# Optimization experiments

Measured on AMD Instinct MI355X. Metric: run time of the kernel, lower is better.

The kernel has to match this reference:

```python
import jax, jax.numpy as jnp
import numpy as np

N = 50000      # num nodes
IN = 256       # in_channels
H = 4          # heads
C = 64         # out_channels per head (concat=False -> out_dim = C)
HOPS = 3       # max_hops == num hops provided
E = 400000     # edges per hop
NEG_SLOPE = 0.2


def setup_inputs() -> dict:
    key = jax.random.key(0)
    ks = jax.random.split(key, 10)
    s_in = 1.0 / np.sqrt(IN)
    s_c = 1.0 / np.sqrt(C)
    return {
        "x": jax.random.normal(ks[0], (N, IN), jnp.float32),
        "ei0": jax.random.randint(ks[1], (2, E), 0, N, dtype=jnp.int32),
        "ei1": jax.random.randint(ks[2], (2, E), 0, N, dtype=jnp.int32),
        "ei2": jax.random.randint(ks[3], (2, E), 0, N, dtype=jnp.int32),
        # shared left/right projections (lin_l / lin_r, shared across hops)
        "W_l": jax.random.normal(ks[4], (IN, H * C), jnp.float32) * s_in,
        "b_l": jnp.zeros((H * C,), jnp.float32),
        "W_r": jax.random.normal(ks[5], (IN, H * C), jnp.float32) * s_in,
        "b_r": jnp.zeros((H * C,), jnp.float32),
        # hop-specific attention vectors and output biases
        "att": jax.random.normal(ks[6], (HOPS, H, C), jnp.float32) * s_c,
        "bias": jnp.zeros((HOPS, C), jnp.float32),
        # hop gate (single Linear since gate_hidden=None)
        "W_gate": jax.random.normal(ks[7], (IN, HOPS), jnp.float32) * s_in,
        "b_gate": jnp.zeros((HOPS,), jnp.float32),
    }


def _segment_softmax(logits, seg, n):
    # logits: [E, H], seg: [E] destination node ids
    m = jax.ops.segment_max(logits, seg, num_segments=n)          # [N, H]
    m = jnp.where(jnp.isfinite(m), m, 0.0)                        # empty segments -> 0
    ex = jnp.exp(logits - m[seg])
    s = jax.ops.segment_sum(ex, seg, num_segments=n)              # [N, H]
    return ex / (s[seg] + 1e-16)


def _gatv2_hop(x_l, x_r, edge_index, att_k, bias_k):
    # x_l, x_r: [N, H, C] shared projections; edge_index: [2, Ek]
    src, dst = edge_index[0], edge_index[1]
    s = jax.nn.leaky_relu(x_l[src] + x_r[dst], NEG_SLOPE)         # [Ek, H, C]
    alpha = jnp.einsum("ehc,hc->eh", s, att_k)                    # [Ek, H]
    alpha = _segment_softmax(alpha, dst, N)
    msg = jax.ops.segment_sum(x_l[src] * alpha[..., None], dst, num_segments=N)  # [N, H, C]
    return msg.mean(axis=1) + bias_k                              # concat=False -> head mean, [N, C]


def reference(x, ei0, ei1, ei2, W_l, b_l, W_r, b_r, att, bias, W_gate, b_gate):
    # shared projections computed once
    x_l = (x @ W_l + b_l).reshape(N, H, C)
    x_r = (x @ W_r + b_r).reshape(N, H, C)

    # hop 0 gets self-loops (add_self_loops=True); higher hops do not
    ar = jnp.arange(N, dtype=ei0.dtype)
    ei0_sl = jnp.concatenate([ei0, jnp.stack([ar, ar])], axis=1)
    edges = [ei0_sl, ei1, ei2]

    messages = jnp.stack(
        [_gatv2_hop(x_l, x_r, edges[k], att[k], bias[k]) for k in range(HOPS)],
        axis=1,
    )  # [N, HOPS, C]

    logits = x @ W_gate + b_gate                                  # [N, HOPS]
    weights = jax.nn.softmax(logits, axis=-1)
    out = jnp.einsum("nkc,nk->nc", messages, weights)             # [N, C]
    return out
```

## Files before the change

kernel.cpp:

```cpp
#include <hip/hip_runtime.h>
#include <math.h>

#define N_NODES 50000
#define IN_DIM 256
#define HEADS 4
#define CDIM 64
#define HC 256
#define HOPS 3
#define EDGES 400000
#define NEG_SLOPE 0.2f
#define SEG (EDGES + N_NODES)
#define TOT_E (3 * EDGES + N_NODES)
#define CAP 32
#define LOG2E 1.44269504f

#define NB_GATE  ((N_NODES + 3) / 4)
#define NB_PACKW ((IN_DIM * 2 * HC) / 256)
#define NB_ZERO  ((HOPS * N_NODES + 255) / 256)
#define NB_SCAT  ((TOT_E + 255) / 256)
#define GB 64
#define AP 264
#define GEMM_BLKS  ((N_NODES + GB - 1) / GB)
#define FUSED_BLKS (GEMM_BLKS + NB_SCAT)

typedef unsigned short ushort;
using short8  = __attribute__((ext_vector_type(8))) short;
using floatx4 = __attribute__((ext_vector_type(4))) float;
using f32x2   = __attribute__((ext_vector_type(2))) float;

__device__ __forceinline__ void decode_flat(int f, int& k, int& e)
{
    if (f < SEG)              { k = 0; e = f; }
    else if (f < SEG + EDGES) { k = 1; e = f - SEG; }
    else                      { k = 2; e = f - SEG - EDGES; }
}

__device__ __forceinline__ ushort f2bf(float f)
{
    unsigned u = __float_as_uint(f);
    unsigned r = u + 0x7fffu + ((u >> 16) & 1u);
    return (ushort)(r >> 16);
}

__device__ __forceinline__ float exp2_raw(float x)
{
    float r;
    asm volatile("v_exp_f32 %0, %1" : "=v"(r) : "v"(x));
    return r;
}

template <int CTRL>
__device__ __forceinline__ float dpp_xadd(float x)
{
    int y = __builtin_amdgcn_update_dpp(
        0, __float_as_int(x), CTRL, 0xF, 0xF, true);
    return x + __int_as_float(y);
}
#define DPP_XOR1 0xB1
#define DPP_XOR2 0x4E
#define DPP_HMIR 0x141

__device__ __forceinline__ f32x2 bf2x(unsigned u)
{
    f32x2 r;
    r.x = __uint_as_float(u << 16);
    r.y = __uint_as_float(u & 0xffff0000u);
    return r;
}

__device__ __forceinline__ f32x2 lrelu2(f32x2 v)
{
    return __builtin_elementwise_max(v, 0.2f * v);
}

__global__ __launch_bounds__(256) void prep_a(
    const float* __restrict__ X, const float* __restrict__ Wg,
    const float* __restrict__ bg, float* __restrict__ gw,
    ushort* __restrict__ Xb,
    const float* __restrict__ Wl, const float* __restrict__ Wr,
    ushort* __restrict__ WT, int* __restrict__ cnt)
{
    const int blk = blockIdx.x;
    const int tid = threadIdx.x;

    if (blk < NB_GATE) {
        const int node = (blk * 256 + tid) >> 6;
        const int lane = tid & 63;
        if (node >= N_NODES) return;

        float4 xv = ((const float4*)(X + (size_t)node * IN_DIM))[lane];

        union { ushort s[4]; uint2 u; } o;
        o.s[0] = f2bf(xv.x); o.s[1] = f2bf(xv.y);
        o.s[2] = f2bf(xv.z); o.s[3] = f2bf(xv.w);
        ((uint2*)(Xb + (size_t)node * IN_DIM))[lane] = o.u;

        float a0 = 0.f, a1 = 0.f, a2 = 0.f;
        const int i0 = lane * 4;
        a0 += xv.x * Wg[(i0 + 0) * HOPS + 0]; a1 += xv.x * Wg[(i0 + 0) * HOPS + 1]; a2 += xv.x * Wg[(i0 + 0) * HOPS + 2];
        a0 += xv.y * Wg[(i0 + 1) * HOPS + 0]; a1 += xv.y * Wg[(i0 + 1) * HOPS + 1]; a2 += xv.y * Wg[(i0 + 1) * HOPS + 2];
        a0 += xv.z * Wg[(i0 + 2) * HOPS + 0]; a1 += xv.z * Wg[(i0 + 2) * HOPS + 1]; a2 += xv.z * Wg[(i0 + 2) * HOPS + 2];
        a0 += xv.w * Wg[(i0 + 3) * HOPS + 0]; a1 += xv.w * Wg[(i0 + 3) * HOPS + 1]; a2 += xv.w * Wg[(i0 + 3) * HOPS + 2];

        #pragma unroll
        for (int off = 32; off >= 1; off >>= 1) {
            a0 += __shfl_xor(a0, off);
            a1 += __shfl_xor(a1, off);
            a2 += __shfl_xor(a2, off);
        }
        if (lane == 0) {
            float l0 = a0 + bg[0], l1 = a1 + bg[1], l2 = a2 + bg[2];
            float m = fmaxf(l0, fmaxf(l1, l2));
            float e0 = expf(l0 - m), e1 = expf(l1 - m), e2 = expf(l2 - m);
            float inv = 1.f / (e0 + e1 + e2);
            gw[node * HOPS + 0] = e0 * inv;
            gw[node * HOPS + 1] = e1 * inv;
            gw[node * HOPS + 2] = e2 * inv;
        }
    } else if (blk < NB_GATE + NB_PACKW) {
        int id = (blk - NB_GATE) * 256 + tid;
        int n = id >> 8;
        int k = id & 255;
        float v = (n < HC) ? Wl[k * HC + n] : Wr[k * HC + (n - HC)];
        WT[(size_t)n * IN_DIM + k] = f2bf(v);
    } else {
        int id = (blk - NB_GATE - NB_PACKW) * 256 + tid;
        if (id < HOPS * N_NODES) cnt[id] = 0;
    }
}

__global__ __launch_bounds__(256, 2) void gemm_scatter(
    const ushort* __restrict__ Xb, const ushort* __restrict__ WT,
    const float* __restrict__ b_l, const float* __restrict__ b_r,
    ushort* __restrict__ xlb, ushort* __restrict__ xrb, int M,
    const int* __restrict__ ei0, const int* __restrict__ ei1,
    const int* __restrict__ ei2, int* __restrict__ cnt,
    ushort* __restrict__ bucket)
{
    __shared__ ushort As[GB][AP];
    const int blk = blockIdx.x;
    const int tid = threadIdx.x;

    if (blk >= GEMM_BLKS) {
        int f = (blk - GEMM_BLKS) * 256 + tid;
        if (f >= TOT_E) return;
        int k, e; decode_flat(f, k, e);
        int s, d;
        if (k == 0 && e >= EDGES) { s = d = e - EDGES; }
        else {
            const int* ei = (k == 0) ? ei0 : (k == 1) ? ei1 : ei2;
            s = ei[e]; d = ei[EDGES + e];
        }
        int pos = atomicAdd(&cnt[k * N_NODES + d], 1);
        if (pos < CAP)
            bucket[((size_t)k * N_NODES + d) * CAP + pos] = (ushort)s;
        return;
    }

    const int wave = tid >> 6, lane = tid & 63;
    const int row0 = blk * GB;
    const int wx   = wave * 128;
    const int lrow = lane & 15, lk = (lane >> 4) * 8;

    #pragma unroll
    for (int j = 0; j < 8; j++) {
        int id = tid + 256 * j;
        int r  = id >> 5;
        int c  = (id & 31) * 8;
        int gr = row0 + r;
        uint4 v = make_uint4(0u, 0u, 0u, 0u);
        if (gr < M)
            v = *(const uint4*)(Xb + (size_t)gr * IN_DIM + c);
        *(uint4*)&As[r][c] = v;
    }
    __syncthreads();

    floatx4 acc[4][8];
    #pragma unroll
    for (int i = 0; i < 4; i++)
        #pragma unroll
        for (int j = 0; j < 8; j++)
            acc[i][j] = (floatx4){0.f, 0.f, 0.f, 0.f};

    #pragma unroll 2
    for (int k0 = 0; k0 < IN_DIM; k0 += 32) {
        short8 af[4], bf[8];
        #pragma unroll
        for (int ni = 0; ni < 8; ni++)
            bf[ni] = *(const short8*)(WT +
                (size_t)(wx + ni * 16 + lrow) * IN_DIM + k0 + lk);
        #pragma unroll
        for (int mi = 0; mi < 4; mi++)
            af[mi] = *(const short8*)&As[mi * 16 + lrow][k0 + lk];

        #pragma unroll
        for (int mi = 0; mi < 4; mi++)
            #pragma unroll
            for (int ni = 0; ni < 8; ni++)
                acc[mi][ni] = __builtin_amdgcn_mfma_f32_16x16x32_bf16(
                    bf[ni], af[mi], acc[mi][ni], 0, 0, 0);
    }

    const int csub = (lane >> 4) * 4;
    const bool left = (wx < HC);
    const float*  bvec = left ? b_l : b_r;
    ushort*       obuf = left ? xlb : xrb;
    const int     cbase = left ? wx : wx - HC;
    #pragma unroll
    for (int mi = 0; mi < 4; mi++) {
        int grow = row0 + mi * 16 + lrow;
        if (grow < M) {
            #pragma unroll
            for (int ni = 0; ni < 8; ni++) {
                int lc = cbase + ni * 16 + csub;
                floatx4 v = acc[mi][ni];
                const float4 b = *(const float4*)(bvec + lc);
                union { ushort s[4]; uint2 u; } o;
                o.s[0] = f2bf(v[0] + b.x);
                o.s[1] = f2bf(v[1] + b.y);
                o.s[2] = f2bf(v[2] + b.z);
                o.s[3] = f2bf(v[3] + b.w);
                *(uint2*)(obuf + (size_t)grow * HC + lc) = o.u;
            }
        }
    }
}

__global__ __launch_bounds__(192) void node_all(
    const ushort* __restrict__ xlb, const ushort* __restrict__ xrb,
    const int* __restrict__ cnt, const ushort* __restrict__ bucket,
    const float* __restrict__ att, const float* __restrict__ gw,
    const float* __restrict__ bias, float* __restrict__ out)
{
    __shared__ float lds[HOPS][CDIM];
    const int n    = blockIdx.x;
    const int k    = threadIdx.x >> 6;
    const int lane = threadIdx.x & 63;
    const int half = lane >> 5;
    const int sub  = lane & 31;
    const unsigned laneoff = (unsigned)sub * 8;

    const int deg = min(cnt[k * N_NODES + n], CAP);
    const ushort* bk = bucket + ((size_t)k * N_NODES + n) * CAP;

    uint4 rq = *(const uint4*)(xrb + (size_t)n * HC + laneoff);
    f32x2 rr[4] = { bf2x(rq.x), bf2x(rq.y), bf2x(rq.z), bf2x(rq.w) };

    const float4 a0 = ((const float4*)(att + (size_t)k * HC))[sub * 2 + 0];
    const float4 a1 = ((const float4*)(att + (size_t)k * HC))[sub * 2 + 1];
    f32x2 w2[4] = { {a0.x * LOG2E, a0.y * LOG2E}, {a0.z * LOG2E, a0.w * LOG2E},
                    {a1.x * LOG2E, a1.y * LOG2E}, {a1.z * LOG2E, a1.w * LOG2E} };

    float denom = 0.f;
    f32x2 acc2[4] = { {0.f,0.f}, {0.f,0.f}, {0.f,0.f}, {0.f,0.f} };

    if (deg > 0) {
        const int degm1 = deg - 1;
        int myS = (lane < deg) ? (int)bk[lane] : 0;
        const int npair = (deg + 1) >> 1;

        int s0 = __shfl(myS, min(half, degm1));
        uint4 q = *(const uint4*)(xlb + (unsigned)s0 * HC + laneoff);

        for (int j = 0; j < npair; j++) {
            int sn = __shfl(myS, min(2 * (j + 1) + half, degm1));
            uint4 qn = *(const uint4*)(xlb + (unsigned)sn * HC + laneoff);

            f32x2 f0 = bf2x(q.x), f1 = bf2x(q.y);
            f32x2 f2 = bf2x(q.z), f3 = bf2x(q.w);

            f32x2 pp = w2[0] * lrelu2(f0 + rr[0]);
            pp = __builtin_elementwise_fma(w2[1], lrelu2(f1 + rr[1]), pp);
            pp = __builtin_elementwise_fma(w2[2], lrelu2(f2 + rr[2]), pp);
            pp = __builtin_elementwise_fma(w2[3], lrelu2(f3 + rr[3]), pp);
            float p = pp.x + pp.y;

            p = dpp_xadd<DPP_XOR1>(p);
            p = dpp_xadd<DPP_XOR2>(p);
            p = dpp_xadd<DPP_HMIR>(p);

            bool valid = (2 * j + half) < deg;
            float ex = valid ? exp2_raw(p) : 0.f;
            denom += ex;
            f32x2 ex2 = { ex, ex };
            acc2[0] = __builtin_elementwise_fma(ex2, f0, acc2[0]);
            acc2[1] = __builtin_elementwise_fma(ex2, f1, acc2[1]);
            acc2[2] = __builtin_elementwise_fma(ex2, f2, acc2[2]);
            acc2[3] = __builtin_elementwise_fma(ex2, f3, acc2[3]);
            q = qn;
        }
    }

    denom += __shfl_xor(denom, 32);
    const float inv = (denom > 0.f) ? 1.f / denom : 0.f;
    const float g   = gw[n * HOPS + k];
    const float* bb = bias + (size_t)k * CDIM + (size_t)(sub & 7) * 8;

    #pragma unroll
    for (int i = 0; i < 4; i++) {
        acc2[i].x += __shfl_xor(acc2[i].x, 32);
        acc2[i].y += __shfl_xor(acc2[i].y, 32);
        acc2[i].x *= inv;
        acc2[i].y *= inv;
        acc2[i].x += __shfl_xor(acc2[i].x, 8);
        acc2[i].y += __shfl_xor(acc2[i].y, 8);
        acc2[i].x += __shfl_xor(acc2[i].x, 16);
        acc2[i].y += __shfl_xor(acc2[i].y, 16);
        if (lane < 8) {
            lds[k][lane * 8 + 2 * i]     = g * (acc2[i].x * 0.25f + bb[2 * i]);
            lds[k][lane * 8 + 2 * i + 1] = g * (acc2[i].y * 0.25f + bb[2 * i + 1]);
        }
    }
    __syncthreads();

    if (threadIdx.x < CDIM)
        out[(size_t)n * CDIM + threadIdx.x] =
            lds[0][threadIdx.x] + lds[1][threadIdx.x] + lds[2][threadIdx.x];
}

extern "C" void kernel_launch(void* const* d_in, const int* in_sizes, int n_in,
                              void* d_out, int out_size, void* d_ws, size_t ws_size,
                              hipStream_t stream)
{
    const float* x      = (const float*)d_in[0];
    const int*   ei0    = (const int*)d_in[1];
    const int*   ei1    = (const int*)d_in[2];
    const int*   ei2    = (const int*)d_in[3];
    const float* W_l    = (const float*)d_in[4];
    const float* b_l    = (const float*)d_in[5];
    const float* W_r    = (const float*)d_in[6];
    const float* b_r    = (const float*)d_in[7];
    const float* att    = (const float*)d_in[8];
    const float* bias   = (const float*)d_in[9];
    const float* W_gate = (const float*)d_in[10];
    const float* b_gate = (const float*)d_in[11];

    const size_t NHC = (size_t)N_NODES * HC;
    float* ws      = (float*)d_ws;
    float* gwbuf   = ws;
    int*   cnt     = (int*)(gwbuf + HOPS * N_NODES);
    ushort* bucket = (ushort*)(cnt + HOPS * N_NODES);
    ushort* xlb    = bucket + (size_t)HOPS * N_NODES * CAP;
    ushort* xrb    = xlb + NHC;
    ushort* Xb     = xrb + NHC;
    ushort* WT     = Xb + NHC;

    prep_a<<<NB_GATE + NB_PACKW + NB_ZERO, 256, 0, stream>>>(
        x, W_gate, b_gate, gwbuf, Xb, W_l, W_r, WT, cnt);

    gemm_scatter<<<FUSED_BLKS, 256, 0, stream>>>(
        Xb, WT, b_l, b_r, xlb, xrb, N_NODES,
        ei0, ei1, ei2, cnt, bucket);

    node_all<<<N_NODES, 192, 0, stream>>>(
        xlb, xrb, cnt, bucket, att, gwbuf, bias, (float*)d_out);
}
```

Baseline: 327.8 us.

## Build per-destination edge buckets in LDS slices instead of global atomics

Edge bucketing moves out of the fused GEMM kernel into its own kernel. Each block owns a slice of destination nodes for one hop, scans every edge of that hop, builds counts and buckets with LDS atomics, then writes the buckets and counts to global memory with coalesced vector stores. This removes global atomics, scattered 2-byte bucket writes and the separate count-zeroing pass. The cost is that every block rereads the whole edge list, only 96 blocks run, and the scatter no longer overlaps with the GEMM.

```diff
diff --git a/kernel.cpp b/kernel.cpp
--- a/kernel.cpp
+++ b/kernel.cpp
@@ -10,30 +10,23 @@
 #define EDGES 400000
 #define NEG_SLOPE 0.2f
 #define SEG (EDGES + N_NODES)
-#define TOT_E (3 * EDGES + N_NODES)
 #define CAP 32
 #define LOG2E 1.44269504f
 
 #define NB_GATE  ((N_NODES + 3) / 4)
 #define NB_PACKW ((IN_DIM * 2 * HC) / 256)
-#define NB_ZERO  ((HOPS * N_NODES + 255) / 256)
-#define NB_SCAT  ((TOT_E + 255) / 256)
+#define NSLICE 32
+#define SLICE_W ((N_NODES + NSLICE - 1) / NSLICE)
+#define SCAT_BLKS (HOPS * NSLICE)
+#define SCAT_THREADS 512
 #define GB 64
 #define AP 264
 #define GEMM_BLKS  ((N_NODES + GB - 1) / GB)
-#define FUSED_BLKS (GEMM_BLKS + NB_SCAT)
 
 typedef unsigned short ushort;
 using short8  = __attribute__((ext_vector_type(8))) short;
 using floatx4 = __attribute__((ext_vector_type(4))) float;
 using f32x2   = __attribute__((ext_vector_type(2))) float;
-
-__device__ __forceinline__ void decode_flat(int f, int& k, int& e)
-{
-    if (f < SEG)              { k = 0; e = f; }
-    else if (f < SEG + EDGES) { k = 1; e = f - SEG; }
-    else                      { k = 2; e = f - SEG - EDGES; }
-}
 
 __device__ __forceinline__ ushort f2bf(float f)
 {
@@ -78,7 +71,7 @@
     const float* __restrict__ bg, float* __restrict__ gw,
     ushort* __restrict__ Xb,
     const float* __restrict__ Wl, const float* __restrict__ Wr,
-    ushort* __restrict__ WT, int* __restrict__ cnt)
+    ushort* __restrict__ WT)
 {
     const int blk = blockIdx.x;
     const int tid = threadIdx.x;
@@ -117,48 +110,64 @@
             gw[node * HOPS + 1] = e1 * inv;
             gw[node * HOPS + 2] = e2 * inv;
         }
-    } else if (blk < NB_GATE + NB_PACKW) {
+    } else {
         int id = (blk - NB_GATE) * 256 + tid;
         int n = id >> 8;
         int k = id & 255;
         float v = (n < HC) ? Wl[k * HC + n] : Wr[k * HC + (n - HC)];
         WT[(size_t)n * IN_DIM + k] = f2bf(v);
-    } else {
-        int id = (blk - NB_GATE - NB_PACKW) * 256 + tid;
-        if (id < HOPS * N_NODES) cnt[id] = 0;
-    }
-}
-
-__global__ __launch_bounds__(256, 2) void gemm_scatter(
-    const ushort* __restrict__ Xb, const ushort* __restrict__ WT,
-    const float* __restrict__ b_l, const float* __restrict__ b_r,
-    ushort* __restrict__ xlb, ushort* __restrict__ xrb, int M,
+    }
+}
+
+__global__ __launch_bounds__(SCAT_THREADS) void scatter_lds(
     const int* __restrict__ ei0, const int* __restrict__ ei1,
     const int* __restrict__ ei2, int* __restrict__ cnt,
     ushort* __restrict__ bucket)
 {
-    __shared__ ushort As[GB][AP];
-    const int blk = blockIdx.x;
-    const int tid = threadIdx.x;
-
-    if (blk >= GEMM_BLKS) {
-        int f = (blk - GEMM_BLKS) * 256 + tid;
-        if (f >= TOT_E) return;
-        int k, e; decode_flat(f, k, e);
+    __shared__ __align__(16) ushort bkt_s[SLICE_W][CAP];
+    __shared__ int cnt_s[SLICE_W];
+    const int k     = blockIdx.x / NSLICE;
+    const int slice = blockIdx.x % NSLICE;
+    const int base  = slice * SLICE_W;
+    const int nn    = min(SLICE_W, N_NODES - base);
+    const int tid   = threadIdx.x;
+
+    for (int i = tid; i < SLICE_W; i += SCAT_THREADS) cnt_s[i] = 0;
+    __syncthreads();
+
+    const int* ei = (k == 0) ? ei0 : (k == 1) ? ei1 : ei2;
+    const int  ne = (k == 0) ? SEG : EDGES;
+    for (int e = tid; e < ne; e += SCAT_THREADS) {
         int s, d;
         if (k == 0 && e >= EDGES) { s = d = e - EDGES; }
-        else {
-            const int* ei = (k == 0) ? ei0 : (k == 1) ? ei1 : ei2;
-            s = ei[e]; d = ei[EDGES + e];
-        }
-        int pos = atomicAdd(&cnt[k * N_NODES + d], 1);
-        if (pos < CAP)
-            bucket[((size_t)k * N_NODES + d) * CAP + pos] = (ushort)s;
-        return;
-    }
-
+        else { s = ei[e]; d = ei[EDGES + e]; }
+        int r = d - base;
+        if ((unsigned)r < (unsigned)nn) {
+            int pos = atomicAdd(&cnt_s[r], 1);
+            if (pos < CAP) bkt_s[r][pos] = (ushort)s;
+        }
+    }
+    __syncthreads();
+
+    for (int i = tid; i < nn; i += SCAT_THREADS)
+        cnt[k * N_NODES + base + i] = cnt_s[i];
+    const int tot_u = nn * CAP;
+    ushort* gdst = bucket + ((size_t)k * N_NODES + base) * CAP;
+    const uint4* ls4 = (const uint4*)&bkt_s[0][0];
+    uint4* gd4 = (uint4*)gdst;
+    const int nv = tot_u >> 3;
+    for (int i = tid; i < nv; i += SCAT_THREADS) gd4[i] = ls4[i];
+}
+
+__global__ __launch_bounds__(256, 2) void gemm_mfma(
+    const ushort* __restrict__ Xb, const ushort* __restrict__ WT,
+    const float* __restrict__ b_l, const float* __restrict__ b_r,
+    ushort* __restrict__ xlb, ushort* __restrict__ xrb, int M)
+{
+    __shared__ ushort As[GB][AP];
+    const int tid  = threadIdx.x;
     const int wave = tid >> 6, lane = tid & 63;
-    const int row0 = blk * GB;
+    const int row0 = blockIdx.x * GB;
     const int wx   = wave * 128;
     const int lrow = lane & 15, lk = (lane >> 4) * 8;
 
@@ -345,12 +354,14 @@
     ushort* Xb     = xrb + NHC;
     ushort* WT     = Xb + NHC;
 
-    prep_a<<<NB_GATE + NB_PACKW + NB_ZERO, 256, 0, stream>>>(
-        x, W_gate, b_gate, gwbuf, Xb, W_l, W_r, WT, cnt);
-
-    gemm_scatter<<<FUSED_BLKS, 256, 0, stream>>>(
-        Xb, WT, b_l, b_r, xlb, xrb, N_NODES,
+    prep_a<<<NB_GATE + NB_PACKW, 256, 0, stream>>>(
+        x, W_gate, b_gate, gwbuf, Xb, W_l, W_r, WT);
+
+    scatter_lds<<<SCAT_BLKS, SCAT_THREADS, 0, stream>>>(
         ei0, ei1, ei2, cnt, bucket);
+
+    gemm_mfma<<<GEMM_BLKS, 256, 0, stream>>>(
+        Xb, WT, b_l, b_r, xlb, xrb, N_NODES);
 
     node_all<<<N_NODES, 192, 0, stream>>>(
         xlb, xrb, cnt, bucket, att, gwbuf, bias, (float*)d_out);
```

Result: slower. 662.9 us (+102.2%).
